# Optimization experiments

Hardware: AMD Instinct MI355X
Metric: run time of the kernel (lower is better)

Reference implementation:

```python
import jax, jax.numpy as jnp
import numpy as np

B, L, D = 8, 8192, 128
H, C = 2, 64          # heads, out_channels = dim // 2; H*C == D so the final view works
N = B * L
E = 1048576
NEG_SLOPE = 0.2


def setup_inputs() -> dict:
    key = jax.random.key(0)
    k1, k2, k3, k4, k5 = jax.random.split(key, 5)
    x = jax.random.normal(k1, (B, L, D), dtype=jnp.float32)
    edge_index = jax.random.randint(k2, (2, E), 0, N, dtype=jnp.int64)
    s = 1.0 / np.sqrt(D)
    W_l = jax.random.uniform(k3, (D, H * C), minval=-s, maxval=s, dtype=jnp.float32)
    W_r = jax.random.uniform(k4, (D, H * C), minval=-s, maxval=s, dtype=jnp.float32)
    att = jax.random.uniform(k5, (H, C), minval=-s, maxval=s, dtype=jnp.float32)
    bias = jnp.zeros((H * C,), dtype=jnp.float32)
    return {"x": x, "edge_index": edge_index, "W_l": W_l, "W_r": W_r, "att": att, "bias": bias}


def reference(x, edge_index, W_l, W_r, att, bias):
    # x: [B, L, D] -> flatten to node features [N, D]
    xf = x.reshape(N, D)
    x_l = (xf @ W_l).reshape(N, H, C)  # source transform
    x_r = (xf @ W_r).reshape(N, H, C)  # target transform

    # add self loops (PyG GATv2Conv default add_self_loops=True)
    loops = jnp.arange(N, dtype=edge_index.dtype)
    src = jnp.concatenate([edge_index[0], loops])  # [E+N]
    dst = jnp.concatenate([edge_index[1], loops])

    # GATv2 attention: e_ij = att . LeakyReLU(x_l[j] + x_r[i])
    feat = jax.nn.leaky_relu(x_l[src] + x_r[dst], NEG_SLOPE)  # [E+N, H, C]
    score = jnp.einsum('ehc,hc->eh', feat, att)               # [E+N, H]

    # segment softmax over incoming edges of each target node
    m = jax.ops.segment_max(score, dst, num_segments=N)       # [N, H]
    num = jnp.exp(score - m[dst])
    den = jax.ops.segment_sum(num, dst, num_segments=N)       # [N, H]
    alpha = num / den[dst]                                    # [E+N, H]

    # weighted aggregation of transformed source features
    out = jax.ops.segment_sum(alpha[:, :, None] * x_l[src], dst, num_segments=N)  # [N, H, C]
    out = out.reshape(N, H * C) + bias
    return out.reshape(B, L, D)
```

## Files before the change

kernel.cpp:

```cpp
#include <hip/hip_runtime.h>

typedef unsigned short u16;
typedef unsigned int   u32;

#define NN     65536
#define DDIM   128
#define EE     1048576
#define NEG_SLOPE 0.2f
#define SUBCAP 640
#define BROW   8192

typedef __attribute__((ext_vector_type(8))) short          short8;
typedef __attribute__((ext_vector_type(2))) float          f32x2;
typedef __attribute__((ext_vector_type(4))) float          f32x4;
typedef __attribute__((ext_vector_type(4))) u32            u32x4;

__device__ __forceinline__ float bf2f(u16 b) { return __uint_as_float(((u32)b) << 16); }
__device__ __forceinline__ u16 f2bf(float f) {
  u32 u = __float_as_uint(f);
  u += 0x7FFFu + ((u >> 16) & 1u);
  return (u16)(u >> 16);
}
__device__ __forceinline__ f32x2 bfp2f(u32 w) {
  f32x2 r;
  r.x = __uint_as_float(w << 16);
  r.y = __uint_as_float(w & 0xFFFF0000u);
  return r;
}
__device__ __forceinline__ f32x2 pk_max(f32x2 a, f32x2 b) {
  f32x2 r; r.x = fmaxf(a.x, b.x); r.y = fmaxf(a.y, b.y); return r;
}

__global__ void init_misc(const int* __restrict__ ei, u32* __restrict__ mode,
                          const float* __restrict__ Wl, const float* __restrict__ Wr,
                          u16* __restrict__ wpack, u32* __restrict__ cursor) {
  int t = threadIdx.x, b = blockIdx.x;
  if (b == 0) {
    if (t < 64) {
      int nz = (ei[2 * t + 1] != 0) ? 1 : 0;
      unsigned long long bal = __ballot(nz);
      if (t == 0) mode[0] = (bal == 0ull) ? 1u : 0u;
    }
    return;
  }
  if (b <= 8) {
    int pb = b - 1;
    int colhalf = pb >> 2, ks = pb & 3;
    int lane = t & 63, pp = t >> 6;
    int m16 = lane & 15, quad = lane >> 4;
#pragma unroll
    for (int pq = 0; pq < 2; ++pq) {
      int p = pq * 4 + pp;
      const float* W = (p < 4) ? Wl : Wr;
      int n = colhalf * 64 + (p & 3) * 16 + m16;
#pragma unroll
      for (int j = 0; j < 8; ++j) {
        int k = ks * 32 + quad * 8 + j;
        wpack[(((((colhalf * 4 + ks) * 8) + p) * 64 + lane) * 8) + j] = f2bf(W[k * DDIM + n]);
      }
    }
    return;
  }
  int i = (b - 9) * 256 + t;
#pragma unroll
  for (int k = 0; k < 16; ++k) cursor[i * 16 + k] = 0;
}

__global__ __launch_bounds__(256) void pass1_bin(const int* __restrict__ ei,
                                                 u32* __restrict__ cursor,
                                                 u32* __restrict__ subb,
                                                 const u32* __restrict__ mode)
{
  __shared__ u32 lcnt[256];
  __shared__ u32 gb[256];
  int pb = blockIdx.x, t = threadIdx.x;
  lcnt[t] = 0;
  __syncthreads();

  int base = (pb * 256 + t) * 8;
  int s[8], d[8];
  if (mode[0]) {
    const long long* ei64 = (const long long*)ei;
#pragma unroll
    for (int k = 0; k < 4; ++k) {
      longlong2 sv = *(const longlong2*)(ei64 + base + 2 * k);
      longlong2 dv = *(const longlong2*)(ei64 + EE + base + 2 * k);
      s[2 * k] = (int)sv.x; s[2 * k + 1] = (int)sv.y;
      d[2 * k] = (int)dv.x; d[2 * k + 1] = (int)dv.y;
    }
  } else {
#pragma unroll
    for (int k = 0; k < 2; ++k) {
      int4 sv = *(const int4*)(ei + base + 4 * k);
      int4 dv = *(const int4*)(ei + EE + base + 4 * k);
      s[4 * k] = sv.x; s[4 * k + 1] = sv.y; s[4 * k + 2] = sv.z; s[4 * k + 3] = sv.w;
      d[4 * k] = dv.x; d[4 * k + 1] = dv.y; d[4 * k + 2] = dv.z; d[4 * k + 3] = dv.w;
    }
  }

  u32 rk[8];
#pragma unroll
  for (int e = 0; e < 8; ++e)
    rk[e] = atomicAdd(&lcnt[(u32)d[e] >> 8], 1u);
  __syncthreads();

  int xs = pb & 7;
  gb[t] = atomicAdd(&cursor[(t * 8 + xs) * 16], lcnt[t]);
  __syncthreads();

#pragma unroll
  for (int e = 0; e < 8; ++e) {
    u32 cell = (u32)d[e] >> 8;
    u32 pos  = gb[cell] + rk[e];
    if (pos < SUBCAP)
      subb[(size_t)(cell * 8 + xs) * SUBCAP + pos] =
          ((u32)(d[e] & 255) << 16) | (u32)s[e];
  }
}

__device__ __forceinline__ void gemm_body(
    int pb, int tid,
    const float* __restrict__ x, const u16* __restrict__ wpack,
    u16* __restrict__ xl, u16* __restrict__ xr)
{
  int wave = tid >> 6;
  int lane = tid & 63;
  int m16  = lane & 15;
  int quad = lane >> 4;
  int mat     = wave >> 1;
  int colhalf = wave & 1;
  int rowbase = pb * 64;

  const u16* wp = wpack + (size_t)colhalf * (4 * 8 * 64 * 8);
  short8 bfr[4][4];
#pragma unroll
  for (int ks = 0; ks < 4; ++ks)
#pragma unroll
    for (int ct = 0; ct < 4; ++ct)
      bfr[ks][ct] = *(const short8*)(wp + ((size_t)(ks * 8 + mat * 4 + ct) * 64 + lane) * 8);

  u16* outp = mat ? xr : xl;
#pragma unroll
  for (int rt = 0; rt < 4; ++rt) {
    int r0 = rowbase + rt * 16;
    f32x4 acc[4] = { {0,0,0,0},{0,0,0,0},{0,0,0,0},{0,0,0,0} };
#pragma unroll
    for (int ks = 0; ks < 4; ++ks) {
      const float* ap = x + (size_t)(r0 + m16) * DDIM + ks * 32 + quad * 8;
      f32x4 a0 = *(const f32x4*)ap;
      f32x4 a1 = *(const f32x4*)(ap + 4);
      short8 a;
#pragma unroll
      for (int c = 0; c < 4; ++c) { a[c] = (short)f2bf(a0[c]); a[4 + c] = (short)f2bf(a1[c]); }
#pragma unroll
      for (int ct = 0; ct < 4; ++ct)
        acc[ct] = __builtin_amdgcn_mfma_f32_16x16x32_bf16(a, bfr[ks][ct], acc[ct], 0, 0, 0);
    }
#pragma unroll
    for (int ct = 0; ct < 4; ++ct) {
      int c = colhalf * 64 + ct * 16 + m16;
#pragma unroll
      for (int rg = 0; rg < 4; ++rg) {
        int r = r0 + quad * 4 + rg;
        outp[(size_t)r * DDIM + c] = f2bf(acc[ct][rg]);
      }
    }
  }
}

__device__ __forceinline__ void pass2_body(
    int b, int t,
    const u32* __restrict__ cursor, const u32* __restrict__ subb,
    u32* __restrict__ rowptr, u16* __restrict__ csr, u32* __restrict__ perm,
    u32* sh, u32* cnt, u32* cbase, u32* hist)
{
  cnt[t] = 0;
  if (t < 64) hist[t] = 0;
  __syncthreads();

  u32 sizes[8];
#pragma unroll
  for (int x = 0; x < 8; ++x) sizes[x] = min(cursor[(b * 8 + x) * 16], (u32)SUBCAP);

  u32 ent[8][3], rk[8][3];
#pragma unroll
  for (int x = 0; x < 8; ++x) {
    const u32* sp = subb + (size_t)(b * 8 + x) * SUBCAP;
#pragma unroll
    for (int r = 0; r < 3; ++r) {
      u32 i = (u32)t + r * 256u;
      ent[x][r] = 0xFFFFFFFFu; rk[x][r] = 0;
      if (i < sizes[x]) {
        u32 e = sp[i];
        ent[x][r] = e;
        rk[x][r]  = atomicAdd(&cnt[e >> 16], 1u);
      }
    }
  }
  __syncthreads();

  u32 c  = cnt[t];
  u32 dc = min(c, 63u);
  u32 pc = (c + 7u) & ~7u;
  atomicAdd(&hist[dc], 1u);
  sh[t] = pc;
  __syncthreads();
  for (int off = 1; off < 256; off <<= 1) {
    u32 v = sh[t]; u32 a = (t >= off) ? sh[t - off] : 0u;
    __syncthreads(); sh[t] = v + a; __syncthreads();
  }
  u32 loc = sh[t] - pc;
  cbase[t] = loc;
  rowptr[b * 256 + t] = ((b * BROW + loc) << 8) | min(c, 255u);
  __syncthreads();
  if (t == 0) {
    u32 run = 0;
    for (int i = 0; i < 64; ++i) { u32 h = hist[i]; hist[i] = run; run += h; }
  }
  __syncthreads();
  u32 r2 = atomicAdd(&hist[dc], 1u);
  perm[b * 256 + r2] = b * 256 + t;
  __syncthreads();

#pragma unroll
  for (int x = 0; x < 8; ++x)
#pragma unroll
    for (int r = 0; r < 3; ++r)
      if (ent[x][r] != 0xFFFFFFFFu) {
        u32 cell = ent[x][r] >> 16;
        csr[b * BROW + cbase[cell] + rk[x][r]] = (u16)(ent[x][r] & 0xFFFFu);
      }
}

__global__ __launch_bounds__(256) void gemm_pass2(
    const float* __restrict__ x, const u16* __restrict__ wpack,
    u16* __restrict__ xl, u16* __restrict__ xr,
    const u32* __restrict__ cursor, const u32* __restrict__ subb,
    u32* __restrict__ rowptr, u16* __restrict__ csr, u32* __restrict__ perm)
{
  __shared__ u32 sh[256];
  __shared__ u32 cnt[256];
  __shared__ u32 cbase[256];
  __shared__ u32 hist[64];
  int b = blockIdx.x;
  if (b < 1024) gemm_body(b, threadIdx.x, x, wpack, xl, xr);
  else          pass2_body(b - 1024, threadIdx.x, cursor, subb,
                           rowptr, csr, perm, sh, cnt, cbase, hist);
}

__device__ __forceinline__ void gat_item(u32x4 xw, const f32x2* av, const f32x2* rv,
                                         float& l, f32x2* acc)
{
  f32x2 xv[4];
  f32x2 sc2 = {0.f, 0.f};
#pragma unroll
  for (int i = 0; i < 4; ++i) {
    xv[i] = bfp2f(xw[i]);
    f32x2 t = xv[i] + rv[i];
    f32x2 lr = pk_max(t, t * NEG_SLOPE);
    sc2 += av[i] * lr;
  }
  float partial = sc2.x + sc2.y;
  partial += __shfl_xor(partial, 1);
  partial += __shfl_xor(partial, 2);
  partial += __shfl_xor(partial, 4);
  float p = __expf(partial);
  l += p;
#pragma unroll
  for (int i = 0; i < 4; ++i) acc[i] += p * xv[i];
}

__global__ __launch_bounds__(256) void gat_fused(
    const u16* __restrict__ xl, const u16* __restrict__ xr,
    const u32* __restrict__ rowptr, const u16* __restrict__ csr,
    const u32* __restrict__ perm,
    const float* __restrict__ att, const float* __restrict__ bias,
    float* __restrict__ out)
{
  int tid    = threadIdx.x;
  int bucket = blockIdx.x & 255;
  int k      = blockIdx.x >> 8;
  int wave   = tid >> 6;
  int wg     = (wave == 0) ? k : (wave == 1) ? (31 - k)
             : (wave == 2) ? (32 + k) : (63 - k);
  int node   = (int)perm[bucket * 256 + wg * 4 + ((tid >> 4) & 3)];
  int q      = tid & 15;
  int c0     = q * 8;
  const u16* __restrict__ xlc = xl + c0;

  u32x4 SW = *(const u32x4*)(xlc + (size_t)node * DDIM);

  f32x2 av[4], rv[4];
  {
    f32x4 a0 = *(const f32x4*)(att + c0);
    f32x4 a1 = *(const f32x4*)(att + c0 + 4);
    av[0].x = a0[0]; av[0].y = a0[1]; av[1].x = a0[2]; av[1].y = a0[3];
    av[2].x = a1[0]; av[2].y = a1[1]; av[3].x = a1[2]; av[3].y = a1[3];
    u32x4 rw = *(const u32x4*)(xr + (size_t)node * DDIM + c0);
#pragma unroll
    for (int i = 0; i < 4; ++i) rv[i] = bfp2f(rw[i]);
  }

  float l = 0.f;
  f32x2 acc[4] = { {0,0},{0,0},{0,0},{0,0} };

  u32 rp  = rowptr[node];
  u32 rs  = rp >> 8;
  int deg = (int)(rp & 255u);
  const u16* __restrict__ cp = csr + rs;

  gat_item(SW, av, rv, l, acc);

  int j = 0;
  while (deg - j >= 16) {
    u32x4 iw0 = *(const u32x4*)(cp + j);
    u32x4 iw1 = *(const u32x4*)(cp + j + 8);
    u32 i0  = iw0.x & 0xFFFFu, i1  = iw0.x >> 16, i2  = iw0.y & 0xFFFFu, i3  = iw0.y >> 16;
    u32 i4  = iw0.z & 0xFFFFu, i5  = iw0.z >> 16, i6  = iw0.w & 0xFFFFu, i7  = iw0.w >> 16;
    u32 i8  = iw1.x & 0xFFFFu, i9  = iw1.x >> 16, i10 = iw1.y & 0xFFFFu, i11 = iw1.y >> 16;
    u32 i12 = iw1.z & 0xFFFFu, i13 = iw1.z >> 16, i14 = iw1.w & 0xFFFFu, i15 = iw1.w >> 16;
    u32x4 L0  = *(const u32x4*)(xlc + (size_t)i0  * DDIM);
    u32x4 L1  = *(const u32x4*)(xlc + (size_t)i1  * DDIM);
    u32x4 L2  = *(const u32x4*)(xlc + (size_t)i2  * DDIM);
    u32x4 L3  = *(const u32x4*)(xlc + (size_t)i3  * DDIM);
    u32x4 L4  = *(const u32x4*)(xlc + (size_t)i4  * DDIM);
    u32x4 L5  = *(const u32x4*)(xlc + (size_t)i5  * DDIM);
    u32x4 L6  = *(const u32x4*)(xlc + (size_t)i6  * DDIM);
    u32x4 L7  = *(const u32x4*)(xlc + (size_t)i7  * DDIM);
    u32x4 L8  = *(const u32x4*)(xlc + (size_t)i8  * DDIM);
    u32x4 L9  = *(const u32x4*)(xlc + (size_t)i9  * DDIM);
    u32x4 L10 = *(const u32x4*)(xlc + (size_t)i10 * DDIM);
    u32x4 L11 = *(const u32x4*)(xlc + (size_t)i11 * DDIM);
    u32x4 L12 = *(const u32x4*)(xlc + (size_t)i12 * DDIM);
    u32x4 L13 = *(const u32x4*)(xlc + (size_t)i13 * DDIM);
    u32x4 L14 = *(const u32x4*)(xlc + (size_t)i14 * DDIM);
    u32x4 L15 = *(const u32x4*)(xlc + (size_t)i15 * DDIM);
    __builtin_amdgcn_sched_barrier(0);
    gat_item(L0,  av, rv, l, acc);
    gat_item(L1,  av, rv, l, acc);
    gat_item(L2,  av, rv, l, acc);
    gat_item(L3,  av, rv, l, acc);
    gat_item(L4,  av, rv, l, acc);
    gat_item(L5,  av, rv, l, acc);
    gat_item(L6,  av, rv, l, acc);
    gat_item(L7,  av, rv, l, acc);
    gat_item(L8,  av, rv, l, acc);
    gat_item(L9,  av, rv, l, acc);
    gat_item(L10, av, rv, l, acc);
    gat_item(L11, av, rv, l, acc);
    gat_item(L12, av, rv, l, acc);
    gat_item(L13, av, rv, l, acc);
    gat_item(L14, av, rv, l, acc);
    gat_item(L15, av, rv, l, acc);
    j += 16;
  }
  if (deg - j >= 8) {
    u32x4 iw = *(const u32x4*)(cp + j);
    u32 i0 = iw.x & 0xFFFFu, i1 = iw.x >> 16, i2 = iw.y & 0xFFFFu, i3 = iw.y >> 16;
    u32 i4 = iw.z & 0xFFFFu, i5 = iw.z >> 16, i6 = iw.w & 0xFFFFu, i7 = iw.w >> 16;
    u32x4 L0 = *(const u32x4*)(xlc + (size_t)i0 * DDIM);
    u32x4 L1 = *(const u32x4*)(xlc + (size_t)i1 * DDIM);
    u32x4 L2 = *(const u32x4*)(xlc + (size_t)i2 * DDIM);
    u32x4 L3 = *(const u32x4*)(xlc + (size_t)i3 * DDIM);
    u32x4 L4 = *(const u32x4*)(xlc + (size_t)i4 * DDIM);
    u32x4 L5 = *(const u32x4*)(xlc + (size_t)i5 * DDIM);
    u32x4 L6 = *(const u32x4*)(xlc + (size_t)i6 * DDIM);
    u32x4 L7 = *(const u32x4*)(xlc + (size_t)i7 * DDIM);
    __builtin_amdgcn_sched_barrier(0);
    gat_item(L0, av, rv, l, acc);
    gat_item(L1, av, rv, l, acc);
    gat_item(L2, av, rv, l, acc);
    gat_item(L3, av, rv, l, acc);
    gat_item(L4, av, rv, l, acc);
    gat_item(L5, av, rv, l, acc);
    gat_item(L6, av, rv, l, acc);
    gat_item(L7, av, rv, l, acc);
    j += 8;
  }
  if (deg - j >= 4) {
    uint2 iw = *(const uint2*)(cp + j);
    u32 i0 = iw.x & 0xFFFFu, i1 = iw.x >> 16, i2 = iw.y & 0xFFFFu, i3 = iw.y >> 16;
    u32x4 L0 = *(const u32x4*)(xlc + (size_t)i0 * DDIM);
    u32x4 L1 = *(const u32x4*)(xlc + (size_t)i1 * DDIM);
    u32x4 L2 = *(const u32x4*)(xlc + (size_t)i2 * DDIM);
    u32x4 L3 = *(const u32x4*)(xlc + (size_t)i3 * DDIM);
    __builtin_amdgcn_sched_barrier(0);
    gat_item(L0, av, rv, l, acc);
    gat_item(L1, av, rv, l, acc);
    gat_item(L2, av, rv, l, acc);
    gat_item(L3, av, rv, l, acc);
    j += 4;
  }
  for (; j < deg; ++j) {
    u32 s = cp[j];
    u32x4 xw = *(const u32x4*)(xlc + (size_t)s * DDIM);
    gat_item(xw, av, rv, l, acc);
  }

  float inv = 1.f / l;
  f32x4 o0, o1;
  o0[0] = fmaf(acc[0].x, inv, bias[c0 + 0]);
  o0[1] = fmaf(acc[0].y, inv, bias[c0 + 1]);
  o0[2] = fmaf(acc[1].x, inv, bias[c0 + 2]);
  o0[3] = fmaf(acc[1].y, inv, bias[c0 + 3]);
  o1[0] = fmaf(acc[2].x, inv, bias[c0 + 4]);
  o1[1] = fmaf(acc[2].y, inv, bias[c0 + 5]);
  o1[2] = fmaf(acc[3].x, inv, bias[c0 + 6]);
  o1[3] = fmaf(acc[3].y, inv, bias[c0 + 7]);
  float* op = out + (size_t)node * DDIM + c0;
  *(f32x4*)op       = o0;
  *(f32x4*)(op + 4) = o1;
}

extern "C" void kernel_launch(void* const* d_in, const int* in_sizes, int n_in,
                              void* d_out, int out_size, void* d_ws, size_t ws_size,
                              hipStream_t stream) {
  (void)in_sizes; (void)n_in; (void)out_size; (void)ws_size;
  const float* x    = (const float*)d_in[0];
  const int*   ei   = (const int*)d_in[1];
  const float* Wl   = (const float*)d_in[2];
  const float* Wr   = (const float*)d_in[3];
  const float* attw = (const float*)d_in[4];
  const float* bias = (const float*)d_in[5];
  float* out = (float*)d_out;

  char* w = (char*)d_ws;
  u16* xl     = (u16*)(w);
  u16* xr     = (u16*)(w + (16u << 20));
  u32* subb   = (u32*)(w + (32u << 20));
  u32* cursor = (u32*)(w + (37u << 20));
  u32* mode   = (u32*)(w + (37u << 20) + (192u << 10));
  u32* rowptr = (u32*)(w + (37u << 20) + (256u << 10));
  u16* csr    = (u16*)(w + (37u << 20) + (512u << 10));
  u16* wpack  = (u16*)(w + (41u << 20) + (512u << 10));
  u32* perm   = (u32*)(w + (41u << 20) + (640u << 10));

  init_misc<<<17, 256, 0, stream>>>(ei, mode, Wl, Wr, wpack, cursor);
  pass1_bin<<<512, 256, 0, stream>>>(ei, cursor, subb, mode);
  gemm_pass2<<<1280, 256, 0, stream>>>(x, wpack, xl, xr, cursor, subb,
                                       rowptr, csr, perm);
  gat_fused<<<NN / 16, 256, 0, stream>>>(xl, xr, rowptr, csr, perm, attw, bias, out);
}
```

Before: 179.7 us.

## Fuse binning, GEMM, CSR build and GAT into persistent kernel with grid barriers

Replaces three separate launches (pass1_bin, gemm_pass2, gat_fused) with one persistent 1024-block kernel that runs each stage and separates them with a software grid-wide barrier (atomic ticket plus generation counter). Work is redistributed so each block bins 1024 edges, then either builds CSR or does one or two GEMM tiles, then processes four GAT units. This aims to remove kernel launch gaps and tail effects between stages. It depends on all 1024 blocks being co-resident (launch_bounds 256,4); otherwise the barrier deadlocks, and barrier spinning adds its own cost.

```diff
diff --git a/kernel.cpp b/kernel.cpp
--- a/kernel.cpp
+++ b/kernel.cpp
@@ -9,6 +9,7 @@
 #define NEG_SLOPE 0.2f
 #define SUBCAP 640
 #define BROW   8192
+#define NBLK   1024
 
 typedef __attribute__((ext_vector_type(8))) short          short8;
 typedef __attribute__((ext_vector_type(2))) float          f32x2;
@@ -31,9 +32,28 @@
   f32x2 r; r.x = fmaxf(a.x, b.x); r.y = fmaxf(a.y, b.y); return r;
 }
 
+__device__ __forceinline__ void gsync(u32* bar) {
+  __syncthreads();
+  if (threadIdx.x == 0) {
+    __threadfence();
+    u32 g = __hip_atomic_load(bar + 1, __ATOMIC_RELAXED, __HIP_MEMORY_SCOPE_AGENT);
+    u32 ticket = __hip_atomic_fetch_add(bar, 1u, __ATOMIC_ACQ_REL, __HIP_MEMORY_SCOPE_AGENT);
+    if (ticket == (u32)NBLK - 1u) {
+      __hip_atomic_store(bar, 0u, __ATOMIC_RELAXED, __HIP_MEMORY_SCOPE_AGENT);
+      __hip_atomic_fetch_add(bar + 1, 1u, __ATOMIC_RELEASE, __HIP_MEMORY_SCOPE_AGENT);
+    } else {
+      while (__hip_atomic_load(bar + 1, __ATOMIC_ACQUIRE, __HIP_MEMORY_SCOPE_AGENT) == g)
+        __builtin_amdgcn_s_sleep(32);
+    }
+    __threadfence();
+  }
+  __syncthreads();
+}
+
 __global__ void init_misc(const int* __restrict__ ei, u32* __restrict__ mode,
                           const float* __restrict__ Wl, const float* __restrict__ Wr,
-                          u16* __restrict__ wpack, u32* __restrict__ cursor) {
+                          u16* __restrict__ wpack, u32* __restrict__ cursor,
+                          u32* __restrict__ bar) {
   int t = threadIdx.x, b = blockIdx.x;
   if (b == 0) {
     if (t < 64) {
@@ -41,6 +61,7 @@
       unsigned long long bal = __ballot(nz);
       if (t == 0) mode[0] = (bal == 0ull) ? 1u : 0u;
     }
+    if (t == 64) { bar[0] = 0u; bar[1] = 0u; }
     return;
   }
   if (b <= 8) {
@@ -66,41 +87,36 @@
   for (int k = 0; k < 16; ++k) cursor[i * 16 + k] = 0;
 }
 
-__global__ __launch_bounds__(256) void pass1_bin(const int* __restrict__ ei,
-                                                 u32* __restrict__ cursor,
-                                                 u32* __restrict__ subb,
-                                                 const u32* __restrict__ mode)
-{
-  __shared__ u32 lcnt[256];
-  __shared__ u32 gb[256];
-  int pb = blockIdx.x, t = threadIdx.x;
+__device__ __forceinline__ void pass1_body(
+    int pb, int t,
+    const int* __restrict__ ei, u32* __restrict__ cursor,
+    u32* __restrict__ subb, u32 md,
+    u32* lcnt, u32* gb)
+{
   lcnt[t] = 0;
   __syncthreads();
 
-  int base = (pb * 256 + t) * 8;
-  int s[8], d[8];
-  if (mode[0]) {
+  int base = (pb * 256 + t) * 4;
+  int s[4], d[4];
+  if (md) {
     const long long* ei64 = (const long long*)ei;
 #pragma unroll
-    for (int k = 0; k < 4; ++k) {
+    for (int k = 0; k < 2; ++k) {
       longlong2 sv = *(const longlong2*)(ei64 + base + 2 * k);
       longlong2 dv = *(const longlong2*)(ei64 + EE + base + 2 * k);
       s[2 * k] = (int)sv.x; s[2 * k + 1] = (int)sv.y;
       d[2 * k] = (int)dv.x; d[2 * k + 1] = (int)dv.y;
     }
   } else {
-#pragma unroll
-    for (int k = 0; k < 2; ++k) {
-      int4 sv = *(const int4*)(ei + base + 4 * k);
-      int4 dv = *(const int4*)(ei + EE + base + 4 * k);
-      s[4 * k] = sv.x; s[4 * k + 1] = sv.y; s[4 * k + 2] = sv.z; s[4 * k + 3] = sv.w;
-      d[4 * k] = dv.x; d[4 * k + 1] = dv.y; d[4 * k + 2] = dv.z; d[4 * k + 3] = dv.w;
-    }
-  }
-
-  u32 rk[8];
-#pragma unroll
-  for (int e = 0; e < 8; ++e)
+    int4 sv = *(const int4*)(ei + base);
+    int4 dv = *(const int4*)(ei + EE + base);
+    s[0] = sv.x; s[1] = sv.y; s[2] = sv.z; s[3] = sv.w;
+    d[0] = dv.x; d[1] = dv.y; d[2] = dv.z; d[3] = dv.w;
+  }
+
+  u32 rk[4];
+#pragma unroll
+  for (int e = 0; e < 4; ++e)
     rk[e] = atomicAdd(&lcnt[(u32)d[e] >> 8], 1u);
   __syncthreads();
 
@@ -109,7 +125,7 @@
   __syncthreads();
 
 #pragma unroll
-  for (int e = 0; e < 8; ++e) {
+  for (int e = 0; e < 4; ++e) {
     u32 cell = (u32)d[e] >> 8;
     u32 pos  = gb[cell] + rk[e];
     if (pos < SUBCAP)
@@ -232,22 +248,6 @@
       }
 }
 
-__global__ __launch_bounds__(256) void gemm_pass2(
-    const float* __restrict__ x, const u16* __restrict__ wpack,
-    u16* __restrict__ xl, u16* __restrict__ xr,
-    const u32* __restrict__ cursor, const u32* __restrict__ subb,
-    u32* __restrict__ rowptr, u16* __restrict__ csr, u32* __restrict__ perm)
-{
-  __shared__ u32 sh[256];
-  __shared__ u32 cnt[256];
-  __shared__ u32 cbase[256];
-  __shared__ u32 hist[64];
-  int b = blockIdx.x;
-  if (b < 1024) gemm_body(b, threadIdx.x, x, wpack, xl, xr);
-  else          pass2_body(b - 1024, threadIdx.x, cursor, subb,
-                           rowptr, csr, perm, sh, cnt, cbase, hist);
-}
-
 __device__ __forceinline__ void gat_item(u32x4 xw, const f32x2* av, const f32x2* rv,
                                          float& l, f32x2* acc)
 {
@@ -270,16 +270,16 @@
   for (int i = 0; i < 4; ++i) acc[i] += p * xv[i];
 }
 
-__global__ __launch_bounds__(256) void gat_fused(
+__device__ __forceinline__ void gat_unit(
+    int u, int tid,
     const u16* __restrict__ xl, const u16* __restrict__ xr,
     const u32* __restrict__ rowptr, const u16* __restrict__ csr,
     const u32* __restrict__ perm,
     const float* __restrict__ att, const float* __restrict__ bias,
     float* __restrict__ out)
 {
-  int tid    = threadIdx.x;
-  int bucket = blockIdx.x & 255;
-  int k      = blockIdx.x >> 8;
+  int bucket = u & 255;
+  int k      = u >> 8;
   int wave   = tid >> 6;
   int wg     = (wave == 0) ? k : (wave == 1) ? (31 - k)
              : (wave == 2) ? (32 + k) : (63 - k);
@@ -412,6 +412,38 @@
   *(f32x4*)(op + 4) = o1;
 }
 
+__global__ __launch_bounds__(256, 4) void mega(
+    const float* __restrict__ x, const int* __restrict__ ei,
+    const float* __restrict__ attw, const float* __restrict__ bias,
+    float* __restrict__ out,
+    u16* __restrict__ xl, u16* __restrict__ xr,
+    u32* __restrict__ subb, u32* __restrict__ cursor, u32* __restrict__ mode,
+    u32* __restrict__ rowptr, u16* __restrict__ csr,
+    u16* __restrict__ wpack, u32* __restrict__ perm, u32* __restrict__ bar)
+{
+  __shared__ u32 smA[256];
+  __shared__ u32 smB[256];
+  __shared__ u32 smC[256];
+  __shared__ u32 smH[64];
+  int b = blockIdx.x, t = threadIdx.x;
+
+  pass1_body(b, t, ei, cursor, subb, mode[0], smA, smB);
+  gsync(bar);
+
+  if (b < 256) {
+    pass2_body(b, t, cursor, subb, rowptr, csr, perm, smA, smB, smC, smH);
+  } else {
+    int g = b - 256;
+    gemm_body(g, t, x, wpack, xl, xr);
+    if (g < 256) gemm_body(768 + g, t, x, wpack, xl, xr);
+  }
+  gsync(bar);
+
+#pragma unroll 1
+  for (int k2 = 0; k2 < 4; ++k2)
+    gat_unit(k2 * 1024 + b, t, xl, xr, rowptr, csr, perm, attw, bias, out);
+}
+
 extern "C" void kernel_launch(void* const* d_in, const int* in_sizes, int n_in,
                               void* d_out, int out_size, void* d_ws, size_t ws_size,
                               hipStream_t stream) {
@@ -430,14 +462,13 @@
   u32* subb   = (u32*)(w + (32u << 20));
   u32* cursor = (u32*)(w + (37u << 20));
   u32* mode   = (u32*)(w + (37u << 20) + (192u << 10));
+  u32* bar    = (u32*)(w + (37u << 20) + (200u << 10));
   u32* rowptr = (u32*)(w + (37u << 20) + (256u << 10));
   u16* csr    = (u16*)(w + (37u << 20) + (512u << 10));
   u16* wpack  = (u16*)(w + (41u << 20) + (512u << 10));
   u32* perm   = (u32*)(w + (41u << 20) + (640u << 10));
 
-  init_misc<<<17, 256, 0, stream>>>(ei, mode, Wl, Wr, wpack, cursor);
-  pass1_bin<<<512, 256, 0, stream>>>(ei, cursor, subb, mode);
-  gemm_pass2<<<1280, 256, 0, stream>>>(x, wpack, xl, xr, cursor, subb,
-                                       rowptr, csr, perm);
-  gat_fused<<<NN / 16, 256, 0, stream>>>(xl, xr, rowptr, csr, perm, attw, bias, out);
-}
+  init_misc<<<17, 256, 0, stream>>>(ei, mode, Wl, Wr, wpack, cursor, bar);
+  mega<<<NBLK, 256, 0, stream>>>(x, ei, attw, bias, out, xl, xr, subb,
+                                 cursor, mode, rowptr, csr, wpack, perm, bar);
+}
```

Result: slower. 615.5 us (+242.4%).
